# Kernel tuning notes

Hardware: AMD Instinct MI355X
Metric: run time of the kernel (lower is better)

Reference implementation:

```python
import jax, jax.numpy as jnp
import numpy as np

EPS = 1e-6

def setup_inputs() -> dict:
    key = jax.random.key(0)
    k1, k2, k3 = jax.random.split(key, 3)
    B, D, V = 8, 4096, 32000
    hidden_states = jax.random.normal(k1, (B, D), dtype=jnp.float32)
    norm_weight = jax.random.normal(k2, (D,), dtype=jnp.float32)
    lm_head_weight = jax.random.normal(k3, (V, D), dtype=jnp.float32) * (D ** -0.5)
    return {"hidden_states": hidden_states, "norm_weight": norm_weight,
            "lm_head_weight": lm_head_weight}

def reference(hidden_states, norm_weight, lm_head_weight):
    # RMSNorm: x * rsqrt(mean(x^2) + eps) * gamma
    var = jnp.mean(jnp.square(hidden_states), axis=-1, keepdims=True)
    h = hidden_states * jax.lax.rsqrt(var + EPS) * norm_weight  # [B, D]
    # vocab projection (GEMV per row): logits [B, V]
    logits = jnp.einsum('bd,vd->bv', h, lm_head_weight)
    # top-1 token, matching torch.topk(logits.float(), 1) -> indices [B, 1]
    token = jnp.argmax(logits.astype(jnp.float32), axis=-1, keepdims=True)
    return token
```

## Files before the change

### kernel.cpp

```cpp
#include <hip/hip_runtime.h>
#include <stdint.h>


#define D 4096
#define BATCH 8
#define VOCAB 32000
#define VT 4
#define NBLK 2000
#define EPS 1e-6f

typedef unsigned long long u64;
typedef float f32x4 __attribute__((ext_vector_type(4)));

__global__ __launch_bounds__(256) void rmsnorm_k(const float* __restrict__ x,
                                                 const float* __restrict__ g,
                                                 float* __restrict__ h) {
    const int b = blockIdx.x;
    const int t = threadIdx.x;
    const int wave = t >> 6, lane = t & 63;
    const float* xr = x + b * D;

    f32x4 xv[4];
    float s = 0.f;
#pragma unroll
    for (int i = 0; i < 4; ++i) {
        xv[i] = *(const f32x4*)(xr + i * 1024 + t * 4);
        s += xv[i].x * xv[i].x + xv[i].y * xv[i].y + xv[i].z * xv[i].z + xv[i].w * xv[i].w;
    }
#pragma unroll
    for (int m = 1; m < 64; m <<= 1) s += __shfl_xor(s, m, 64);

    __shared__ float wsum[4];
    if (lane == 0) wsum[wave] = s;
    __syncthreads();
    const float tot = wsum[0] + wsum[1] + wsum[2] + wsum[3];
    const float rs = rsqrtf(tot * (1.f / (float)D) + EPS);

#pragma unroll
    for (int i = 0; i < 4; ++i) {
        const int d = i * 1024 + t * 4;
        const f32x4 gv = *(const f32x4*)(g + d);
        f32x4 o;
        o.x = xv[i].x * rs * gv.x;
        o.y = xv[i].y * rs * gv.y;
        o.z = xv[i].z * rs * gv.z;
        o.w = xv[i].w * rs * gv.w;
        *(f32x4*)(h + b * D + d) = o;
    }
}

__global__ __launch_bounds__(256) void gemv_argmax_k(const float* __restrict__ W,
                                                     const float* __restrict__ h,
                                                     u64* __restrict__ partial) {
    const int lane = threadIdx.x & 63;
    const int wave = threadIdx.x >> 6;
    const int grp = blockIdx.x * 4 + wave;
    const int v0 = grp * VT;
    const float* Wb = W + (size_t)v0 * D;
    const int dl = lane * 4;

    float acc[32];
#pragma unroll
    for (int i = 0; i < 32; ++i) acc[i] = 0.f;

    f32x4 wA[VT], wB[VT];
    f32x4 hA[8], hB[8];

#define LOADH(HB, c)                                                           \
    {                                                                          \
        const int _d = (c) * 256 + dl;                                         \
        _Pragma("unroll")                                                      \
        for (int b = 0; b < 8; ++b)                                            \
            HB[b] = *(const f32x4*)(h + b * D + _d);                           \
    }

#define LOADW(BUF, c)                                                          \
    {                                                                          \
        const int _d = (c) * 256 + dl;                                         \
        _Pragma("unroll")                                                      \
        for (int vi = 0; vi < VT; ++vi)                                        \
            BUF[vi] = *(const f32x4*)(Wb + vi * D + _d);                       \
    }

#define COMPUTE(HB, WBUF)                                                      \
    {                                                                          \
        _Pragma("unroll")                                                      \
        for (int b = 0; b < 8; ++b) {                                          \
            _Pragma("unroll")                                                  \
            for (int vi = 0; vi < VT; ++vi)                                    \
                acc[b * VT + vi] += WBUF[vi].x * HB[b].x + WBUF[vi].y * HB[b].y + \
                                    WBUF[vi].z * HB[b].z + WBUF[vi].w * HB[b].w;  \
        }                                                                      \
    }

    LOADH(hA, 0)
    LOADW(wA, 0)
#pragma unroll 1
    for (int c = 0; c <= 12; c += 2) {
        LOADH(hB, c + 1)
        LOADW(wB, c + 1)
        COMPUTE(hA, wA)
        LOADH(hA, c + 2)
        LOADW(wA, c + 2)
        COMPUTE(hB, wB)
    }
    LOADH(hB, 15)
    LOADW(wB, 15)
    COMPUTE(hA, wA)
    COMPUTE(hB, wB)
#undef LOADH
#undef LOADW
#undef COMPUTE

#pragma unroll
    for (int s = 0; s < 5; ++s) {
        const int m = 1 << s;
        const bool bit = (lane & m) != 0;
#pragma unroll
        for (int u = 0; u < (32 >> (s + 1)); ++u) {
            const float a = acc[2 * u];
            const float c2 = acc[2 * u + 1];
            const float keep = bit ? c2 : a;
            const float send = bit ? a : c2;
            acc[u] = keep + __shfl_xor(send, m, 64);
        }
    }
    const float logit = acc[0] + __shfl_xor(acc[0], 32, 64);

    const int vidx = v0 + (lane & 3);
    const uint32_t fb = __float_as_uint(logit);
    const uint32_t key = (fb & 0x80000000u) ? ~fb : (fb | 0x80000000u);
    u64 best = ((u64)key << 32) | (uint32_t)(~(uint32_t)vidx);

#pragma unroll
    for (int m = 1; m <= 2; m <<= 1) {
        const u64 o = __shfl_xor(best, m, 64);
        if (o > best) best = o;
    }
    {
        const u64 o = __shfl_xor(best, 32, 64);
        if (o > best) best = o;
    }

    __shared__ u64 lb[4][8];
    if (lane < 32 && (lane & 3) == 0) lb[wave][lane >> 2] = best;
    __syncthreads();
    if (threadIdx.x < 8) {
        const u64 m0 = lb[0][threadIdx.x], m1 = lb[1][threadIdx.x];
        const u64 m2 = lb[2][threadIdx.x], m3 = lb[3][threadIdx.x];
        const u64 a = m0 > m1 ? m0 : m1;
        const u64 b2 = m2 > m3 ? m2 : m3;
        partial[(size_t)blockIdx.x * 8 + threadIdx.x] = a > b2 ? a : b2;
    }
}

__global__ __launch_bounds__(512) void finalize_k(const u64* __restrict__ partial,
                                                  int* __restrict__ out, int nblk) {
    const int b = threadIdx.x >> 6;
    const int lane = threadIdx.x & 63;
    u64 best = 0ull;
    for (int p = lane; p < nblk; p += 64) {
        const u64 x = partial[(size_t)p * 8 + b];
        if (x > best) best = x;
    }
#pragma unroll
    for (int m = 1; m < 64; m <<= 1) {
        const u64 o = __shfl_xor(best, m, 64);
        if (o > best) best = o;
    }
    if (lane == 0) out[b] = (int)(~(uint32_t)best);
}

extern "C" void kernel_launch(void* const* d_in, const int* in_sizes, int n_in,
                              void* d_out, int out_size, void* d_ws, size_t ws_size,
                              hipStream_t stream) {
    const float* x = (const float*)d_in[0];
    const float* g = (const float*)d_in[1];
    const float* W = (const float*)d_in[2];
    int* out = (int*)d_out;

    float* h = (float*)d_ws;
    u64* partial = (u64*)((char*)d_ws + BATCH * D * sizeof(float));

    rmsnorm_k<<<BATCH, 256, 0, stream>>>(x, g, h);
    gemv_argmax_k<<<NBLK, 256, 0, stream>>>(W, h, partial);
    finalize_k<<<1, 512, 0, stream>>>(partial, out, NBLK);
}
```

Measured before the change: 133.8 us.

## Stream weight tiles into LDS via global_load_lds with manual vmcnt waits

Weight rows are now fetched with direct global-to-LDS loads into a double-buffered shared array, and each wave reads them back from LDS before the FMA loop. Explicit s_waitcnt vmcnt(12) and sched barriers replace compiler-inserted waits, so the hidden-state loads stay in flight while compute runs. The aim is to cut vector register pressure and let more loads stay outstanding. The cost is an extra LDS read per tile and reliance on hand-counted vmcnt values matching the number of issued loads.

```diff
diff --git a/kernel.cpp b/kernel.cpp
--- a/kernel.cpp
+++ b/kernel.cpp
@@ -11,6 +11,8 @@
 
 typedef unsigned long long u64;
 typedef float f32x4 __attribute__((ext_vector_type(4)));
+
+#define SB __builtin_amdgcn_sched_barrier(0)
 
 __global__ __launch_bounds__(256) void rmsnorm_k(const float* __restrict__ x,
                                                  const float* __restrict__ g,
@@ -52,10 +54,10 @@
 __global__ __launch_bounds__(256) void gemv_argmax_k(const float* __restrict__ W,
                                                      const float* __restrict__ h,
                                                      u64* __restrict__ partial) {
+    __shared__ float wbuf[2][16][256];
     const int lane = threadIdx.x & 63;
     const int wave = threadIdx.x >> 6;
-    const int grp = blockIdx.x * 4 + wave;
-    const int v0 = grp * VT;
+    const int v0 = blockIdx.x * 16 + wave * VT;
     const float* Wb = W + (size_t)v0 * D;
     const int dl = lane * 4;
 
@@ -63,7 +65,6 @@
 #pragma unroll
     for (int i = 0; i < 32; ++i) acc[i] = 0.f;
 
-    f32x4 wA[VT], wB[VT];
     f32x4 hA[8], hB[8];
 
 #define LOADH(HB, c)                                                           \
@@ -74,43 +75,58 @@
             HB[b] = *(const f32x4*)(h + b * D + _d);                           \
     }
 
-#define LOADW(BUF, c)                                                          \
-    {                                                                          \
-        const int _d = (c) * 256 + dl;                                         \
-        _Pragma("unroll")                                                      \
-        for (int vi = 0; vi < VT; ++vi)                                        \
-            BUF[vi] = *(const f32x4*)(Wb + vi * D + _d);                       \
-    }
-
-#define COMPUTE(HB, WBUF)                                                      \
+#define DMA(p, c)                                                              \
     {                                                                          \
         _Pragma("unroll")                                                      \
-        for (int b = 0; b < 8; ++b) {                                          \
+        for (int vi = 0; vi < VT; ++vi) {                                      \
+            const float* _src = Wb + (size_t)vi * D + (c) * 256 + dl;          \
+            __builtin_amdgcn_global_load_lds(                                  \
+                (const __attribute__((address_space(1))) void*)_src,           \
+                (__attribute__((address_space(3))) void*)&wbuf[p][wave * VT + vi][0], \
+                16, 0, 0);                                                     \
+        }                                                                      \
+    }
+
+#define COMPUTE(HB, p)                                                         \
+    {                                                                          \
+        _Pragma("unroll")                                                      \
+        for (int vi = 0; vi < VT; ++vi) {                                      \
+            const f32x4 wv = *(const f32x4*)&wbuf[p][wave * VT + vi][dl];      \
             _Pragma("unroll")                                                  \
-            for (int vi = 0; vi < VT; ++vi)                                    \
-                acc[b * VT + vi] += WBUF[vi].x * HB[b].x + WBUF[vi].y * HB[b].y + \
-                                    WBUF[vi].z * HB[b].z + WBUF[vi].w * HB[b].w;  \
+            for (int b = 0; b < 8; ++b)                                        \
+                acc[b * VT + vi] += wv.x * HB[b].x + wv.y * HB[b].y +          \
+                                    wv.z * HB[b].z + wv.w * HB[b].w;           \
         }                                                                      \
     }
 
+#define WAIT12  SB; asm volatile("s_waitcnt vmcnt(12)" ::: "memory"); SB;
+#define WAIT0   SB; asm volatile("s_waitcnt vmcnt(0)" ::: "memory"); SB;
+
     LOADH(hA, 0)
-    LOADW(wA, 0)
+    DMA(0, 0)
+
 #pragma unroll 1
     for (int c = 0; c <= 12; c += 2) {
         LOADH(hB, c + 1)
-        LOADW(wB, c + 1)
-        COMPUTE(hA, wA)
+        DMA(1, c + 1)
+        WAIT12
+        COMPUTE(hA, 0)
         LOADH(hA, c + 2)
-        LOADW(wA, c + 2)
-        COMPUTE(hB, wB)
+        DMA(0, c + 2)
+        WAIT12
+        COMPUTE(hB, 1)
     }
     LOADH(hB, 15)
-    LOADW(wB, 15)
-    COMPUTE(hA, wA)
-    COMPUTE(hB, wB)
+    DMA(1, 15)
+    WAIT12
+    COMPUTE(hA, 0)
+    WAIT0
+    COMPUTE(hB, 1)
 #undef LOADH
-#undef LOADW
+#undef DMA
 #undef COMPUTE
+#undef WAIT12
+#undef WAIT0
 
 #pragma unroll
     for (int s = 0; s < 5; ++s) {
```

Result: no change. 131.5 us (-1.7%).
